# Performance work log

Hardware: AMD Instinct MI355X
Metric: run time of the kernel (lower is better)

## Reference

```python
import jax, jax.numpy as jnp
import numpy as np

N_NODES = 100000
N_EDGES = 1600000
IN_F, HID_F, OUT_F = 128, 128, 64


def _sage_conv(x, src, dst, W_self, W_neigh, b, n_nodes):
    # DGL SAGEConv 'mean': out = x @ W_self + mean_{u in N(v)} x_u @ W_neigh + b
    agg = jax.ops.segment_sum(x[src], dst, num_segments=n_nodes)  # [N, d]
    deg = jax.ops.segment_sum(jnp.ones_like(dst, dtype=x.dtype), dst, num_segments=n_nodes)
    neigh = agg / jnp.maximum(deg, 1.0)[:, None]  # zero-in-degree nodes -> 0
    return x @ W_self + neigh @ W_neigh + b


def setup_inputs() -> dict:
    key = jax.random.key(0)
    ks = jax.random.split(key, 8)
    return {
        "features": jax.random.normal(ks[0], (N_NODES, IN_F), dtype=jnp.float32),
        "edge_src": jax.random.randint(ks[1], (N_EDGES,), 0, N_NODES, dtype=jnp.int32),
        "edge_dst": jax.random.randint(ks[2], (N_EDGES,), 0, N_NODES, dtype=jnp.int32),
        "W1_self": jax.random.normal(ks[3], (IN_F, HID_F), dtype=jnp.float32) / np.sqrt(IN_F),
        "W1_neigh": jax.random.normal(ks[4], (IN_F, HID_F), dtype=jnp.float32) / np.sqrt(IN_F),
        "b1": jnp.zeros((HID_F,), dtype=jnp.float32),
        "W2_self": jax.random.normal(ks[5], (HID_F, OUT_F), dtype=jnp.float32) / np.sqrt(HID_F),
        "W2_neigh": jax.random.normal(ks[6], (HID_F, OUT_F), dtype=jnp.float32) / np.sqrt(HID_F),
        "b2": jnp.zeros((OUT_F,), dtype=jnp.float32),
    }


def reference(features, edge_src, edge_dst, W1_self, W1_neigh, b1, W2_self, W2_neigh, b2):
    n = features.shape[0]
    x = _sage_conv(features, edge_src, edge_dst, W1_self, W1_neigh, b1, n)
    x = jax.nn.relu(x)
    # dropout with training=False is a no-op
    return _sage_conv(x, edge_src, edge_dst, W2_self, W2_neigh, b2, n)
```

## Files before the change

kernel.cpp:

```cpp
#include <hip/hip_runtime.h>

#define NODES 100000
#define EDGES 1600000
#define BSH 8
#define NBUCK ((NODES + 255) >> BSH)
#define CHUNK 4096
#define LMAX 8192
#define MCHUNKS ((NODES + 31) / 32)
#define CONVB 12500
#define MLPGRID 512

using bf16x8 = __attribute__((ext_vector_type(8))) short;
using f32x4  = __attribute__((ext_vector_type(4))) float;
using f32x2  = __attribute__((ext_vector_type(2))) float;

__device__ __forceinline__ unsigned short f2b(float f) {
    unsigned u = __builtin_bit_cast(unsigned, f);
    unsigned r = (u + 0x7FFFu + ((u >> 16) & 1u)) >> 16;
    return (unsigned short)r;
}

__device__ __forceinline__ f32x2 pkadd(f32x2 a, f32x2 b) {
    f32x2 d;
    asm("v_pk_add_f32 %0, %1, %2" : "=v"(d) : "v"(a), "v"(b));
    return d;
}
__device__ __forceinline__ f32x2 pkfma(f32x2 a, f32x2 b, f32x2 c) {
    f32x2 d;
    asm("v_pk_fma_f32 %0, %1, %2, %3" : "=v"(d) : "v"(a), "v"(b), "v"(c));
    return d;
}
__device__ __forceinline__ unsigned cvt2bf(float lo, float hi) {
    unsigned r;
    asm("v_cvt_pk_bf16_f32 %0, %1, %2" : "=v"(r) : "v"(lo), "v"(hi));
    return r;
}

__device__ __forceinline__ bf16x8 gl16(const unsigned short* p) {
    bf16x8 r;
    asm volatile("global_load_dwordx4 %0, %1, off" : "=&v"(r) : "v"(p));
    return r;
}

__device__ __forceinline__ void addpk8(f32x2* a, uint2 v) {
    a[0] = pkadd(a[0], __builtin_amdgcn_cvt_pk_f32_fp8((int)v.x, false));
    a[1] = pkadd(a[1], __builtin_amdgcn_cvt_pk_f32_fp8((int)v.x, true));
    a[2] = pkadd(a[2], __builtin_amdgcn_cvt_pk_f32_fp8((int)v.y, false));
    a[3] = pkadd(a[3], __builtin_amdgcn_cvt_pk_f32_fp8((int)v.y, true));
}


__global__ __launch_bounds__(256) void conv_hist(
    const float* __restrict__ in, unsigned short* __restrict__ outb,
    unsigned char* __restrict__ outq, int n4,
    const float* __restrict__ W1s, const float* __restrict__ W1n,
    const float* __restrict__ W2s, const float* __restrict__ W2n,
    unsigned short* __restrict__ Wt1s, unsigned short* __restrict__ Wt1n,
    unsigned short* __restrict__ Wt2s, unsigned short* __restrict__ Wt2n,
    const int* __restrict__ dst, int* __restrict__ bucket_cnt) {
    int t = threadIdx.x;
    if (blockIdx.x < CONVB) {
        int i = blockIdx.x * 256 + t;
        if (i < n4) {
            float4 v = reinterpret_cast<const float4*>(in)[i];
            uint2 o;
            o.x = (unsigned)f2b(v.x) | ((unsigned)f2b(v.y) << 16);
            o.y = (unsigned)f2b(v.z) | ((unsigned)f2b(v.w) << 16);
            reinterpret_cast<uint2*>(outb)[i] = o;
            int pk = __builtin_amdgcn_cvt_pk_fp8_f32(v.x, v.y, 0, false);
            pk = __builtin_amdgcn_cvt_pk_fp8_f32(v.z, v.w, pk, true);
            reinterpret_cast<unsigned*>(outq)[i] = (unsigned)pk;
        }
        if (i < 16384) {
            int k = i >> 7, n = i & 127;
            Wt1s[n * 128 + k] = f2b(W1s[i]);
            Wt1n[n * 128 + k] = f2b(W1n[i]);
        }
        if (i < 8192) {
            int k = i >> 6, n = i & 63;
            Wt2s[n * 128 + k] = f2b(W2s[i]);
            Wt2n[n * 128 + k] = f2b(W2n[i]);
        }
        return;
    }
    __shared__ int lcnt[512];
    lcnt[t] = 0; lcnt[t + 256] = 0;
    __syncthreads();
    int base = (blockIdx.x - CONVB) * 16384;
    int n = EDGES - base;
    if (n > 16384) n = 16384;
    const int4* d4 = reinterpret_cast<const int4*>(dst + base);
    for (int i = t; i < (n >> 2); i += 256) {
        int4 d = d4[i];
        atomicAdd(&lcnt[d.x >> BSH], 1);
        atomicAdd(&lcnt[d.y >> BSH], 1);
        atomicAdd(&lcnt[d.z >> BSH], 1);
        atomicAdd(&lcnt[d.w >> BSH], 1);
    }
    for (int i = (n & ~3) + t; i < n; i += 256) atomicAdd(&lcnt[dst[base + i] >> BSH], 1);
    __syncthreads();
    if (lcnt[t]) atomicAdd(&bucket_cnt[t], lcnt[t]);
    if (lcnt[t + 256]) atomicAdd(&bucket_cnt[t + 256], lcnt[t + 256]);
}

__global__ void bscan_kernel(const int* __restrict__ bucket_cnt, int* __restrict__ bucket_off,
                             int* __restrict__ gcursor, int* __restrict__ row_ptr) {
    __shared__ int sh[512];
    int t = threadIdx.x;
    int v = (t < NBUCK) ? bucket_cnt[t] : 0;
    sh[t] = v;
    __syncthreads();
    for (int off = 1; off < 512; off <<= 1) {
        int x = (t >= off) ? sh[t - off] : 0;
        __syncthreads();
        sh[t] += x;
        __syncthreads();
    }
    int excl = sh[t] - v;
    if (t < NBUCK) { bucket_off[t] = excl; gcursor[t] = excl; }
    if (t == NBUCK) bucket_off[t] = EDGES;
    if (t == 0) row_ptr[NODES] = EDGES;
}

__global__ __launch_bounds__(256) void binscat_kernel(
    const int* __restrict__ src, const int* __restrict__ dst,
    int* __restrict__ gcursor, unsigned* __restrict__ pairs) {
    __shared__ int cnt[512];
    __shared__ int scn[512];
    __shared__ int gbs[512];
    __shared__ int cur[512];
    __shared__ uint2 stage[CHUNK];
    int t = threadIdx.x;
    int base = blockIdx.x * CHUNK;
    int n = EDGES - base;
    if (n > CHUNK) n = CHUNK;

    cnt[t] = 0; cnt[t + 256] = 0;
    __syncthreads();

    uint2 my[16];
#pragma unroll
    for (int i = 0; i < 16; ++i) {
        int idx = t + i * 256;
        if (idx < n) {
            int d = dst[base + idx];
            int s = src[base + idx];
            my[i] = make_uint2((unsigned)d, (unsigned)s);
            atomicAdd(&cnt[d >> BSH], 1);
        } else {
            my[i] = make_uint2(0xFFFFFFFFu, 0);
        }
    }
    __syncthreads();
    scn[t] = cnt[t]; scn[t + 256] = cnt[t + 256];
    __syncthreads();
    for (int off = 1; off < 512; off <<= 1) {
        int a0 = (t >= off) ? scn[t - off] : 0;
        int a1 = (t + 256 >= off) ? scn[t + 256 - off] : 0;
        __syncthreads();
        scn[t] += a0; scn[t + 256] += a1;
        __syncthreads();
    }
    cur[t] = scn[t] - cnt[t];
    cur[t + 256] = scn[t + 256] - cnt[t + 256];
    __syncthreads();
#pragma unroll
    for (int i = 0; i < 16; ++i) {
        if (my[i].x != 0xFFFFFFFFu) {
            int b = (int)(my[i].x >> BSH);
            int p = atomicAdd(&cur[b], 1);
            stage[p] = my[i];
        }
    }
    for (int b2 = t; b2 < 512; b2 += 256) {
        int c = cnt[b2];
        gbs[b2] = (c > 0 && b2 < NBUCK) ? atomicAdd(&gcursor[b2], c) : 0;
    }
    __syncthreads();
    for (int idx = t; idx < n; idx += 256) {
        uint2 p = stage[idx];
        int b = (int)(p.x >> BSH);
        int excl = scn[b] - cnt[b];
        pairs[gbs[b] + idx - excl] = ((p.x & 255u) << 24) | p.y;
    }
}

__global__ __launch_bounds__(256) void localsort_kernel(
    const unsigned* __restrict__ pairs, const int* __restrict__ bucket_off,
    int* __restrict__ row_ptr, int* __restrict__ src_sorted) {
    __shared__ int cnt[256];
    __shared__ int cur[256];
    __shared__ int stage[LMAX];
    int b = blockIdx.x;
    int t = threadIdx.x;
    int node0 = b << BSH;
    int pbeg = bucket_off[b], pend = bucket_off[b + 1];
    int n = pend - pbeg;
    cnt[t] = 0;
    __syncthreads();
    for (int e = pbeg + t; e < pend; e += 256)
        atomicAdd(&cnt[(int)(pairs[e] >> 24)], 1);
    __syncthreads();
    int v = cnt[t];
    cur[t] = v;
    __syncthreads();
    for (int off = 1; off < 256; off <<= 1) {
        int x = (t >= off) ? cur[t - off] : 0;
        __syncthreads();
        cur[t] += x;
        __syncthreads();
    }
    int excl = cur[t] - v;
    int node = node0 + t;
    if (node < NODES) row_ptr[node] = pbeg + excl;
    cur[t] = excl;
    __syncthreads();
    if (n <= LMAX) {
        for (int e = pbeg + t; e < pend; e += 256) {
            unsigned p = pairs[e];
            int pos = atomicAdd(&cur[(int)(p >> 24)], 1);
            stage[pos] = (int)(p & 0xFFFFFFu);
        }
        __syncthreads();
        for (int i = t; i < n; i += 256) src_sorted[pbeg + i] = stage[i];
    } else {
        for (int e = pbeg + t; e < pend; e += 256) {
            unsigned p = pairs[e];
            int pos = atomicAdd(&cur[(int)(p >> 24)], 1);
            src_sorted[pbeg + pos] = (int)(p & 0xFFFFFFu);
        }
    }
}


__global__ __launch_bounds__(256) void agg128_fp8(
    const unsigned char* __restrict__ xq, const int* __restrict__ row_ptr,
    const int* __restrict__ srcs, unsigned short* __restrict__ out) {
    int wave = (blockIdx.x * 256 + threadIdx.x) >> 6;
    int lane = threadIdx.x & 63;
    int sl = lane & 15;
    int n = wave * 4 + (lane >> 4);
    if (n >= NODES) return;
    int beg = row_ptr[n], end = row_ptr[n + 1];
    int gb = lane & 48;

    f32x2 A0[4], A1[4];
#pragma unroll
    for (int i = 0; i < 4; ++i) { A0[i] = {0.f, 0.f}; A1[i] = {0.f, 0.f}; }

    const unsigned char* xs = xq + sl * 8;
    for (int base = beg; base < end; base += 16) {
        int idx = base + sl;
        int sv = (idx < end) ? srcs[idx] : NODES;
        uint2 vv[8], ww[8];
#pragma unroll
        for (int j = 0; j < 8; ++j) {
            int s = __shfl(sv, gb + j, 64);
            vv[j] = *reinterpret_cast<const uint2*>(xs + (size_t)s * 128);
        }
#pragma unroll
        for (int j = 0; j < 8; ++j) {
            int s = __shfl(sv, gb + 8 + j, 64);
            ww[j] = *reinterpret_cast<const uint2*>(xs + (size_t)s * 128);
        }
#pragma unroll
        for (int j = 0; j < 8; ++j) addpk8((j & 1) ? A1 : A0, vv[j]);
#pragma unroll
        for (int j = 0; j < 8; ++j) addpk8((j & 1) ? A0 : A1, ww[j]);
    }

    float inv = 1.0f / fmaxf((float)(end - beg), 1.0f);
    f32x2 iv = {inv, inv};
    f32x2 z = {0.f, 0.f};
    f32x2 r0 = pkfma(pkadd(A0[0], A1[0]), iv, z);
    f32x2 r1 = pkfma(pkadd(A0[1], A1[1]), iv, z);
    f32x2 r2 = pkfma(pkadd(A0[2], A1[2]), iv, z);
    f32x2 r3 = pkfma(pkadd(A0[3], A1[3]), iv, z);
    uint4 o;
    o.x = cvt2bf(r0[0], r0[1]);
    o.y = cvt2bf(r1[0], r1[1]);
    o.z = cvt2bf(r2[0], r2[1]);
    o.w = cvt2bf(r3[0], r3[1]);
    *reinterpret_cast<uint4*>(out + (size_t)n * 128 + sl * 8) = o;
}

__global__ __launch_bounds__(256) void agg64_add8(
    const unsigned char* __restrict__ xq, const int* __restrict__ row_ptr,
    const int* __restrict__ srcs, float* __restrict__ out) {
    int wave = (blockIdx.x * 256 + threadIdx.x) >> 6;
    int lane = threadIdx.x & 63;
    int sl = lane & 7;
    int n = wave * 8 + (lane >> 3);
    if (n >= NODES) return;
    int beg = row_ptr[n], end = row_ptr[n + 1];
    int gb = lane & 56;

    f32x2 A0[4], A1[4];
#pragma unroll
    for (int i = 0; i < 4; ++i) { A0[i] = {0.f, 0.f}; A1[i] = {0.f, 0.f}; }

    const unsigned char* xs = xq + sl * 8;
    for (int base = beg; base < end; base += 8) {
        int idx = base + sl;
        int sv = (idx < end) ? srcs[idx] : NODES;
        uint2 vv[8];
#pragma unroll
        for (int j = 0; j < 8; ++j) {
            int s = __shfl(sv, gb + j, 64);
            vv[j] = *reinterpret_cast<const uint2*>(xs + (size_t)s * 64);
        }
#pragma unroll
        for (int j = 0; j < 8; ++j) addpk8((j & 1) ? A1 : A0, vv[j]);
    }

    float inv = 1.0f / fmaxf((float)(end - beg), 1.0f);
    f32x2 iv = {inv, inv};
    float* op = out + (size_t)n * 64 + sl * 8;
    f32x2 r0 = *reinterpret_cast<f32x2*>(op);
    f32x2 r1 = *reinterpret_cast<f32x2*>(op + 2);
    f32x2 r2 = *reinterpret_cast<f32x2*>(op + 4);
    f32x2 r3 = *reinterpret_cast<f32x2*>(op + 6);
    r0 = pkfma(pkadd(A0[0], A1[0]), iv, r0);
    r1 = pkfma(pkadd(A0[1], A1[1]), iv, r1);
    r2 = pkfma(pkadd(A0[2], A1[2]), iv, r2);
    r3 = pkfma(pkadd(A0[3], A1[3]), iv, r3);
    *reinterpret_cast<f32x2*>(op) = r0;
    *reinterpret_cast<f32x2*>(op + 2) = r1;
    *reinterpret_cast<f32x2*>(op + 4) = r2;
    *reinterpret_cast<f32x2*>(op + 6) = r3;
}


__global__ __launch_bounds__(256, 2) void fused_mlp(
    const unsigned short* __restrict__ featb, const unsigned short* __restrict__ agg,
    const unsigned short* __restrict__ Wt1s, const unsigned short* __restrict__ Wt1n,
    const float* __restrict__ b1, const unsigned short* __restrict__ Wt2s,
    const unsigned short* __restrict__ Wt2n, const float* __restrict__ b2,
    unsigned char* __restrict__ x1h8, float* __restrict__ outp) {
    __shared__ __align__(16) unsigned short w1t[32768];
    __shared__ __align__(16) unsigned short x1t[32 * 136];
    int wid = threadIdx.x >> 6, lane = threadIdx.x & 63;
    int l15 = lane & 15, quad = lane >> 4;

    {
        const uint4* gs = reinterpret_cast<const uint4*>(Wt1s);
        const uint4* gn = reinterpret_cast<const uint4*>(Wt1n);
        uint4* ls = reinterpret_cast<uint4*>(w1t);
        uint4* ln = reinterpret_cast<uint4*>(w1t) + 2048;
#pragma unroll
        for (int i = 0; i < 8; ++i) {
            int g = threadIdx.x + i * 256;
            int sw = (g & ~15) | ((g & 15) ^ ((g >> 4) & 7));
            ls[sw] = gs[g];
            ln[sw] = gn[g];
        }
    }

    int col2 = wid * 16 + l15;
    bf16x8 B2s[4], B2n[4];
#pragma unroll
    for (int k = 0; k < 4; ++k) {
        B2s[k] = gl16(Wt2s + (size_t)col2 * 128 + k * 32 + quad * 8);
        B2n[k] = gl16(Wt2n + (size_t)col2 * 128 + k * 32 + quad * 8);
    }
    float bv1[2];
    bv1[0] = b1[wid * 32 + l15];
    bv1[1] = b1[wid * 32 + 16 + l15];
    float bv2 = b2[col2];

    auto loadA = [&](int cc, bf16x8 (&Afd)[2][4], bf16x8 (&Aad)[2][4]) {
#pragma unroll
        for (int rg = 0; rg < 2; ++rg) {
            int r = cc * 32 + rg * 16 + l15;
            const unsigned short* fp = featb + (size_t)r * 128 + quad * 8;
            const unsigned short* ap = agg + (size_t)r * 128 + quad * 8;
#pragma unroll
            for (int k = 0; k < 4; ++k) {
                Afd[rg][k] = *reinterpret_cast<const bf16x8*>(fp + k * 32);
                Aad[rg][k] = *reinterpret_cast<const bf16x8*>(ap + k * 32);
            }
        }
    };

    bf16x8 Af[2][4], Aa[2][4];
    int c = blockIdx.x;
    if (c < MCHUNKS) loadA(c, Af, Aa);

    asm volatile("s_waitcnt vmcnt(0)" ::: "memory");
    __builtin_amdgcn_sched_barrier(0);
    __syncthreads();

    int swz = l15 & 7;
    const unsigned short* wb0 = w1t + (size_t)(wid * 32 + l15) * 128;
    const unsigned short* wb1 = w1t + (size_t)(wid * 32 + 16 + l15) * 128;

    for (; c < MCHUNKS; c += MLPGRID) {
        int rbase = c * 32;
        int cn = c + MLPGRID;

        f32x4 acc[2][2];
#pragma unroll
        for (int rg = 0; rg < 2; ++rg)
#pragma unroll
            for (int nt = 0; nt < 2; ++nt) acc[rg][nt] = {0.f, 0.f, 0.f, 0.f};
#pragma unroll
        for (int k = 0; k < 4; ++k) {
            int so = ((k * 4 + quad) ^ swz) << 3;
            bf16x8 b1s0 = *reinterpret_cast<const bf16x8*>(wb0 + so);
            bf16x8 b1n0 = *reinterpret_cast<const bf16x8*>(wb0 + 16384 + so);
            bf16x8 b1s1 = *reinterpret_cast<const bf16x8*>(wb1 + so);
            bf16x8 b1n1 = *reinterpret_cast<const bf16x8*>(wb1 + 16384 + so);
#pragma unroll
            for (int rg = 0; rg < 2; ++rg) {
                acc[rg][0] = __builtin_amdgcn_mfma_f32_16x16x32_bf16(Af[rg][k], b1s0, acc[rg][0], 0, 0, 0);
                acc[rg][0] = __builtin_amdgcn_mfma_f32_16x16x32_bf16(Aa[rg][k], b1n0, acc[rg][0], 0, 0, 0);
                acc[rg][1] = __builtin_amdgcn_mfma_f32_16x16x32_bf16(Af[rg][k], b1s1, acc[rg][1], 0, 0, 0);
                acc[rg][1] = __builtin_amdgcn_mfma_f32_16x16x32_bf16(Aa[rg][k], b1n1, acc[rg][1], 0, 0, 0);
            }
        }

        bf16x8 Pf[2][4], Pa[2][4];
        if (cn < MCHUNKS) loadA(cn, Pf, Pa);

#pragma unroll
        for (int nt = 0; nt < 2; ++nt)
#pragma unroll
            for (int rg = 0; rg < 2; ++rg)
#pragma unroll
                for (int rr = 0; rr < 4; ++rr) {
                    float v = fmaxf(acc[rg][nt][rr] + bv1[nt], 0.f);
                    x1t[(rg * 16 + quad * 4 + rr) * 136 + wid * 32 + nt * 16 + l15] = f2b(v);
                }
        __syncthreads();

        f32x4 acc2s[2], acc2n[2];
#pragma unroll
        for (int rg = 0; rg < 2; ++rg) { acc2s[rg] = {0.f, 0.f, 0.f, 0.f}; acc2n[rg] = {0.f, 0.f, 0.f, 0.f}; }
#pragma unroll
        for (int k = 0; k < 4; ++k)
#pragma unroll
            for (int rg = 0; rg < 2; ++rg) {
                bf16x8 a = *reinterpret_cast<const bf16x8*>(&x1t[(rg * 16 + l15) * 136 + k * 32 + quad * 8]);
                acc2s[rg] = __builtin_amdgcn_mfma_f32_16x16x32_bf16(a, B2s[k], acc2s[rg], 0, 0, 0);
                acc2n[rg] = __builtin_amdgcn_mfma_f32_16x16x32_bf16(a, B2n[k], acc2n[rg], 0, 0, 0);
            }
        __syncthreads();

#pragma unroll
        for (int rg = 0; rg < 2; ++rg)
#pragma unroll
            for (int rr = 0; rr < 4; ++rr) {
                int row = rbase + rg * 16 + quad * 4 + rr;
                float vn = acc2n[rg][rr];
                int pk = __builtin_amdgcn_cvt_pk_fp8_f32(vn, vn, 0, false);
                x1h8[(size_t)row * 64 + col2] = (unsigned char)(pk & 0xFF);
                outp[(size_t)row * 64 + col2] = acc2s[rg][rr] + bv2;
            }

        if (cn < MCHUNKS) {
#pragma unroll
            for (int rg = 0; rg < 2; ++rg)
#pragma unroll
                for (int k = 0; k < 4; ++k) {
                    Af[rg][k] = Pf[rg][k];
                    Aa[rg][k] = Pa[rg][k];
                }
        }
    }
}


extern "C" void kernel_launch(void* const* d_in, const int* in_sizes, int n_in,
                              void* d_out, int out_size, void* d_ws, size_t ws_size,
                              hipStream_t stream) {
    const float* features = (const float*)d_in[0];
    const int* esrc = (const int*)d_in[1];
    const int* edst = (const int*)d_in[2];
    const float* W1s = (const float*)d_in[3];
    const float* W1n = (const float*)d_in[4];
    const float* b1  = (const float*)d_in[5];
    const float* W2s = (const float*)d_in[6];
    const float* W2n = (const float*)d_in[7];
    const float* b2  = (const float*)d_in[8];
    float* out = (float*)d_out;

    char* ws = (char*)d_ws;
    size_t off = 0;
    auto alloc = [&](size_t bytes) {
        void* p = ws + off;
        off += (bytes + 255) & ~(size_t)255;
        return p;
    };
    int* bucket_cnt = (int*)alloc(512 * 4);
    int* bucket_off = (int*)alloc(512 * 4);
    int* gcursor    = (int*)alloc(512 * 4);
    int* row_ptr    = (int*)alloc((size_t)(NODES + 1) * 4);
    int* src_sorted = (int*)alloc((size_t)EDGES * 4);
    unsigned* pairs = (unsigned*)alloc((size_t)EDGES * 4);
    unsigned short* featb = (unsigned short*)alloc((size_t)NODES * 128 * 2);
    unsigned char*  feat8 = (unsigned char*)alloc((size_t)(NODES + 1) * 128);
    unsigned short* agg1  = (unsigned short*)alloc((size_t)NODES * 128 * 2);
    unsigned char*  x1h8  = (unsigned char*)alloc((size_t)(NODES + 1) * 64);
    unsigned short* Wt1s  = (unsigned short*)alloc(16384 * 2);
    unsigned short* Wt1n  = (unsigned short*)alloc(16384 * 2);
    unsigned short* Wt2s  = (unsigned short*)alloc(8192 * 2);
    unsigned short* Wt2n  = (unsigned short*)alloc(8192 * 2);

    hipMemsetAsync(bucket_cnt, 0, 512 * 4, stream);
    hipMemsetAsync(feat8 + (size_t)NODES * 128, 0, 128, stream);
    hipMemsetAsync(x1h8 + (size_t)NODES * 64, 0, 64, stream);

    conv_hist<<<CONVB + (EDGES + 16383) / 16384, 256, 0, stream>>>(
        features, featb, feat8, NODES * 128 / 4, W1s, W1n, W2s, W2n,
        Wt1s, Wt1n, Wt2s, Wt2n, edst, bucket_cnt);

    bscan_kernel<<<1, 512, 0, stream>>>(bucket_cnt, bucket_off, gcursor, row_ptr);
    binscat_kernel<<<(EDGES + CHUNK - 1) / CHUNK, 256, 0, stream>>>(esrc, edst, gcursor, pairs);
    localsort_kernel<<<NBUCK, 256, 0, stream>>>(pairs, bucket_off, row_ptr, src_sorted);

    agg128_fp8<<<(NODES / 4 * 64 + 255) / 256, 256, 0, stream>>>(feat8, row_ptr, src_sorted, agg1);

    fused_mlp<<<MLPGRID, 256, 0, stream>>>(featb, agg1, Wt1s, Wt1n, b1, Wt2s, Wt2n, b2, x1h8, out);

    agg64_add8<<<(NODES / 8 * 64 + 255) / 256, 256, 0, stream>>>(x1h8, row_ptr, src_sorted, out);
}
```

Before: 255.8 us.

## Split fused two-layer MLP kernel into separate layer kernels via global bf16 buffer

Splits the fused MLP kernel into two kernels. The first computes the layer-1 hidden activations and writes them to a new global bf16 buffer. The second reads that buffer, computes the layer-2 self and neighbor projections, and prefetches the next chunk in registers. This removes the shared-memory round trip and the block barriers inside the loop, and lets the second layer use a larger grid and higher occupancy. In exchange it adds an extra ~25MB of global write and read traffic plus one more kernel launch.

```diff
diff --git a/kernel.cpp b/kernel.cpp
--- a/kernel.cpp
+++ b/kernel.cpp
@@ -8,7 +8,8 @@
 #define LMAX 8192
 #define MCHUNKS ((NODES + 31) / 32)
 #define CONVB 12500
-#define MLPGRID 512
+#define MLP1GRID 512
+#define MLP2GRID 1024
 
 using bf16x8 = __attribute__((ext_vector_type(8))) short;
 using f32x4  = __attribute__((ext_vector_type(4))) float;
@@ -331,14 +332,11 @@
 }
 
 
-__global__ __launch_bounds__(256, 2) void fused_mlp(
+__global__ __launch_bounds__(256, 2) void mlp1(
     const unsigned short* __restrict__ featb, const unsigned short* __restrict__ agg,
     const unsigned short* __restrict__ Wt1s, const unsigned short* __restrict__ Wt1n,
-    const float* __restrict__ b1, const unsigned short* __restrict__ Wt2s,
-    const unsigned short* __restrict__ Wt2n, const float* __restrict__ b2,
-    unsigned char* __restrict__ x1h8, float* __restrict__ outp) {
+    const float* __restrict__ b1, unsigned short* __restrict__ x1b) {
     __shared__ __align__(16) unsigned short w1t[32768];
-    __shared__ __align__(16) unsigned short x1t[32 * 136];
     int wid = threadIdx.x >> 6, lane = threadIdx.x & 63;
     int l15 = lane & 15, quad = lane >> 4;
 
@@ -355,18 +353,9 @@
             ln[sw] = gn[g];
         }
     }
-
-    int col2 = wid * 16 + l15;
-    bf16x8 B2s[4], B2n[4];
-#pragma unroll
-    for (int k = 0; k < 4; ++k) {
-        B2s[k] = gl16(Wt2s + (size_t)col2 * 128 + k * 32 + quad * 8);
-        B2n[k] = gl16(Wt2n + (size_t)col2 * 128 + k * 32 + quad * 8);
-    }
     float bv1[2];
     bv1[0] = b1[wid * 32 + l15];
     bv1[1] = b1[wid * 32 + 16 + l15];
-    float bv2 = b2[col2];
 
     auto loadA = [&](int cc, bf16x8 (&Afd)[2][4], bf16x8 (&Aad)[2][4]) {
 #pragma unroll
@@ -385,18 +374,15 @@
     bf16x8 Af[2][4], Aa[2][4];
     int c = blockIdx.x;
     if (c < MCHUNKS) loadA(c, Af, Aa);
-
-    asm volatile("s_waitcnt vmcnt(0)" ::: "memory");
-    __builtin_amdgcn_sched_barrier(0);
     __syncthreads();
 
     int swz = l15 & 7;
     const unsigned short* wb0 = w1t + (size_t)(wid * 32 + l15) * 128;
     const unsigned short* wb1 = w1t + (size_t)(wid * 32 + 16 + l15) * 128;
 
-    for (; c < MCHUNKS; c += MLPGRID) {
+    for (; c < MCHUNKS; c += MLP1GRID) {
         int rbase = c * 32;
-        int cn = c + MLPGRID;
+        int cn = c + MLP1GRID;
 
         f32x4 acc[2][2];
 #pragma unroll
@@ -429,9 +415,59 @@
 #pragma unroll
                 for (int rr = 0; rr < 4; ++rr) {
                     float v = fmaxf(acc[rg][nt][rr] + bv1[nt], 0.f);
-                    x1t[(rg * 16 + quad * 4 + rr) * 136 + wid * 32 + nt * 16 + l15] = f2b(v);
+                    int row = rbase + rg * 16 + quad * 4 + rr;
+                    x1b[(size_t)row * 128 + wid * 32 + nt * 16 + l15] = f2b(v);
                 }
-        __syncthreads();
+
+        if (cn < MCHUNKS) {
+#pragma unroll
+            for (int rg = 0; rg < 2; ++rg)
+#pragma unroll
+                for (int k = 0; k < 4; ++k) {
+                    Af[rg][k] = Pf[rg][k];
+                    Aa[rg][k] = Pa[rg][k];
+                }
+        }
+    }
+}
+
+
+__global__ __launch_bounds__(256, 3) void mlp2(
+    const unsigned short* __restrict__ x1b,
+    const unsigned short* __restrict__ Wt2s, const unsigned short* __restrict__ Wt2n,
+    const float* __restrict__ b2,
+    unsigned char* __restrict__ x1h8, float* __restrict__ outp) {
+    int wid = threadIdx.x >> 6, lane = threadIdx.x & 63;
+    int l15 = lane & 15, quad = lane >> 4;
+    int col2 = wid * 16 + l15;
+
+    bf16x8 B2s[4], B2n[4];
+#pragma unroll
+    for (int k = 0; k < 4; ++k) {
+        B2s[k] = gl16(Wt2s + (size_t)col2 * 128 + k * 32 + quad * 8);
+        B2n[k] = gl16(Wt2n + (size_t)col2 * 128 + k * 32 + quad * 8);
+    }
+    float bv2 = b2[col2];
+    asm volatile("s_waitcnt vmcnt(0)" ::: "memory");
+    __builtin_amdgcn_sched_barrier(0);
+
+    auto loadA = [&](int cc, bf16x8 (&Ad)[2][4]) {
+#pragma unroll
+        for (int rg = 0; rg < 2; ++rg) {
+            int r = cc * 32 + rg * 16 + l15;
+            const unsigned short* xp = x1b + (size_t)r * 128 + quad * 8;
+#pragma unroll
+            for (int k = 0; k < 4; ++k) Ad[rg][k] = *reinterpret_cast<const bf16x8*>(xp + k * 32);
+        }
+    };
+
+    bf16x8 A[2][4];
+    int c = blockIdx.x;
+    if (c < MCHUNKS) loadA(c, A);
+
+    for (; c < MCHUNKS; c += MLP2GRID) {
+        int rbase = c * 32;
+        int cn = c + MLP2GRID;
 
         f32x4 acc2s[2], acc2n[2];
 #pragma unroll
@@ -440,11 +476,12 @@
         for (int k = 0; k < 4; ++k)
 #pragma unroll
             for (int rg = 0; rg < 2; ++rg) {
-                bf16x8 a = *reinterpret_cast<const bf16x8*>(&x1t[(rg * 16 + l15) * 136 + k * 32 + quad * 8]);
-                acc2s[rg] = __builtin_amdgcn_mfma_f32_16x16x32_bf16(a, B2s[k], acc2s[rg], 0, 0, 0);
-                acc2n[rg] = __builtin_amdgcn_mfma_f32_16x16x32_bf16(a, B2n[k], acc2n[rg], 0, 0, 0);
+                acc2s[rg] = __builtin_amdgcn_mfma_f32_16x16x32_bf16(A[rg][k], B2s[k], acc2s[rg], 0, 0, 0);
+                acc2n[rg] = __builtin_amdgcn_mfma_f32_16x16x32_bf16(A[rg][k], B2n[k], acc2n[rg], 0, 0, 0);
             }
-        __syncthreads();
+
+        bf16x8 P[2][4];
+        if (cn < MCHUNKS) loadA(cn, P);
 
 #pragma unroll
         for (int rg = 0; rg < 2; ++rg)
@@ -461,10 +498,7 @@
 #pragma unroll
             for (int rg = 0; rg < 2; ++rg)
 #pragma unroll
-                for (int k = 0; k < 4; ++k) {
-                    Af[rg][k] = Pf[rg][k];
-                    Aa[rg][k] = Pa[rg][k];
-                }
+                for (int k = 0; k < 4; ++k) A[rg][k] = P[rg][k];
         }
     }
 }
@@ -500,6 +534,7 @@
     unsigned short* featb = (unsigned short*)alloc((size_t)NODES * 128 * 2);
     unsigned char*  feat8 = (unsigned char*)alloc((size_t)(NODES + 1) * 128);
     unsigned short* agg1  = (unsigned short*)alloc((size_t)NODES * 128 * 2);
+    unsigned short* x1b   = (unsigned short*)alloc((size_t)NODES * 128 * 2);
     unsigned char*  x1h8  = (unsigned char*)alloc((size_t)(NODES + 1) * 64);
     unsigned short* Wt1s  = (unsigned short*)alloc(16384 * 2);
     unsigned short* Wt1n  = (unsigned short*)alloc(16384 * 2);
@@ -520,7 +555,8 @@
 
     agg128_fp8<<<(NODES / 4 * 64 + 255) / 256, 256, 0, stream>>>(feat8, row_ptr, src_sorted, agg1);
 
-    fused_mlp<<<MLPGRID, 256, 0, stream>>>(featb, agg1, Wt1s, Wt1n, b1, Wt2s, Wt2n, b2, x1h8, out);
+    mlp1<<<MLP1GRID, 256, 0, stream>>>(featb, agg1, Wt1s, Wt1n, b1, x1b);
+    mlp2<<<MLP2GRID, 256, 0, stream>>>(x1b, Wt2s, Wt2n, b2, x1h8, out);
 
     agg64_add8<<<(NODES / 8 * 64 + 255) / 256, 256, 0, stream>>>(x1h8, row_ptr, src_sorted, out);
 }
```

Result: slower. 267.2 us (+4.5%).

## Retile fused MLP to 64-row chunks and unroll gather loop by 16 edges

Applied to the files above, without the earlier changes.

The fused MLP now processes 64-row chunks. Each wave owns 16 rows and computes all 128 hidden columns, where before the wave split by column over 32 rows. The x1 LDS tile uses an XOR swizzle in place of padding, and tail rows are clamped or guarded. The layer-2 aggregation gathers 16 neighbours per iteration so more loads are in flight. In exchange, each wave reads more weight data from LDS per MFMA and uses more registers, which may lower occupancy.

```diff
diff --git a/kernel.cpp b/kernel.cpp
--- a/kernel.cpp
+++ b/kernel.cpp
@@ -6,7 +6,7 @@
 #define NBUCK ((NODES + 255) >> BSH)
 #define CHUNK 4096
 #define LMAX 8192
-#define MCHUNKS ((NODES + 31) / 32)
+#define NCH64 ((NODES + 63) / 64)
 #define CONVB 12500
 #define MLPGRID 512
 
@@ -300,17 +300,23 @@
     for (int i = 0; i < 4; ++i) { A0[i] = {0.f, 0.f}; A1[i] = {0.f, 0.f}; }
 
     const unsigned char* xs = xq + sl * 8;
-    for (int base = beg; base < end; base += 8) {
-        int idx = base + sl;
-        int sv = (idx < end) ? srcs[idx] : NODES;
-        uint2 vv[8];
+    for (int base = beg; base < end; base += 16) {
+        int i0 = base + sl, i1 = base + 8 + sl;
+        int sv0 = (i0 < end) ? srcs[i0] : NODES;
+        int sv1 = (i1 < end) ? srcs[i1] : NODES;
+        uint2 vv[16];
 #pragma unroll
         for (int j = 0; j < 8; ++j) {
-            int s = __shfl(sv, gb + j, 64);
+            int s = __shfl(sv0, gb + j, 64);
             vv[j] = *reinterpret_cast<const uint2*>(xs + (size_t)s * 64);
         }
 #pragma unroll
-        for (int j = 0; j < 8; ++j) addpk8((j & 1) ? A1 : A0, vv[j]);
+        for (int j = 0; j < 8; ++j) {
+            int s = __shfl(sv1, gb + j, 64);
+            vv[8 + j] = *reinterpret_cast<const uint2*>(xs + (size_t)s * 64);
+        }
+#pragma unroll
+        for (int j = 0; j < 16; ++j) addpk8((j & 1) ? A1 : A0, vv[j]);
     }
 
     float inv = 1.0f / fmaxf((float)(end - beg), 1.0f);
@@ -338,7 +344,7 @@
     const unsigned short* __restrict__ Wt2n, const float* __restrict__ b2,
     unsigned char* __restrict__ x1h8, float* __restrict__ outp) {
     __shared__ __align__(16) unsigned short w1t[32768];
-    __shared__ __align__(16) unsigned short x1t[32 * 136];
+    __shared__ __align__(16) unsigned short x1t[64 * 128];
     int wid = threadIdx.x >> 6, lane = threadIdx.x & 63;
     int l15 = lane & 15, quad = lane >> 4;
 
@@ -346,7 +352,7 @@
         const uint4* gs = reinterpret_cast<const uint4*>(Wt1s);
         const uint4* gn = reinterpret_cast<const uint4*>(Wt1n);
         uint4* ls = reinterpret_cast<uint4*>(w1t);
-        uint4* ln = reinterpret_cast<uint4*>(w1t) + 2048;
+        uint4* ln = ls + 2048;
 #pragma unroll
         for (int i = 0; i < 8; ++i) {
             int g = threadIdx.x + i * 256;
@@ -363,108 +369,102 @@
         B2s[k] = gl16(Wt2s + (size_t)col2 * 128 + k * 32 + quad * 8);
         B2n[k] = gl16(Wt2n + (size_t)col2 * 128 + k * 32 + quad * 8);
     }
-    float bv1[2];
-    bv1[0] = b1[wid * 32 + l15];
-    bv1[1] = b1[wid * 32 + 16 + l15];
     float bv2 = b2[col2];
-
-    auto loadA = [&](int cc, bf16x8 (&Afd)[2][4], bf16x8 (&Aad)[2][4]) {
-#pragma unroll
-        for (int rg = 0; rg < 2; ++rg) {
-            int r = cc * 32 + rg * 16 + l15;
-            const unsigned short* fp = featb + (size_t)r * 128 + quad * 8;
-            const unsigned short* ap = agg + (size_t)r * 128 + quad * 8;
-#pragma unroll
-            for (int k = 0; k < 4; ++k) {
-                Afd[rg][k] = *reinterpret_cast<const bf16x8*>(fp + k * 32);
-                Aad[rg][k] = *reinterpret_cast<const bf16x8*>(ap + k * 32);
-            }
+    float bv1[8];
+#pragma unroll
+    for (int nt = 0; nt < 8; ++nt) bv1[nt] = b1[nt * 16 + l15];
+
+    auto loadA = [&](int cc, bf16x8 (&Afd)[4], bf16x8 (&Aad)[4]) {
+        int r = cc * 64 + wid * 16 + l15;
+        if (r >= NODES) r = NODES - 1;
+        const unsigned short* fp = featb + (size_t)r * 128 + quad * 8;
+        const unsigned short* ap = agg + (size_t)r * 128 + quad * 8;
+#pragma unroll
+        for (int k = 0; k < 4; ++k) {
+            Afd[k] = *reinterpret_cast<const bf16x8*>(fp + k * 32);
+            Aad[k] = *reinterpret_cast<const bf16x8*>(ap + k * 32);
         }
     };
 
-    bf16x8 Af[2][4], Aa[2][4];
+    bf16x8 Af[4], Aa[4];
     int c = blockIdx.x;
-    if (c < MCHUNKS) loadA(c, Af, Aa);
+    if (c < NCH64) loadA(c, Af, Aa);
 
     asm volatile("s_waitcnt vmcnt(0)" ::: "memory");
     __builtin_amdgcn_sched_barrier(0);
     __syncthreads();
 
     int swz = l15 & 7;
-    const unsigned short* wb0 = w1t + (size_t)(wid * 32 + l15) * 128;
-    const unsigned short* wb1 = w1t + (size_t)(wid * 32 + 16 + l15) * 128;
-
-    for (; c < MCHUNKS; c += MLPGRID) {
-        int rbase = c * 32;
+
+    for (; c < NCH64; c += MLPGRID) {
+        int rbase = c * 64;
         int cn = c + MLPGRID;
 
-        f32x4 acc[2][2];
-#pragma unroll
-        for (int rg = 0; rg < 2; ++rg)
-#pragma unroll
-            for (int nt = 0; nt < 2; ++nt) acc[rg][nt] = {0.f, 0.f, 0.f, 0.f};
+        f32x4 acc[8];
+#pragma unroll
+        for (int nt = 0; nt < 8; ++nt) acc[nt] = {0.f, 0.f, 0.f, 0.f};
 #pragma unroll
         for (int k = 0; k < 4; ++k) {
             int so = ((k * 4 + quad) ^ swz) << 3;
-            bf16x8 b1s0 = *reinterpret_cast<const bf16x8*>(wb0 + so);
-            bf16x8 b1n0 = *reinterpret_cast<const bf16x8*>(wb0 + 16384 + so);
-            bf16x8 b1s1 = *reinterpret_cast<const bf16x8*>(wb1 + so);
-            bf16x8 b1n1 = *reinterpret_cast<const bf16x8*>(wb1 + 16384 + so);
-#pragma unroll
-            for (int rg = 0; rg < 2; ++rg) {
-                acc[rg][0] = __builtin_amdgcn_mfma_f32_16x16x32_bf16(Af[rg][k], b1s0, acc[rg][0], 0, 0, 0);
-                acc[rg][0] = __builtin_amdgcn_mfma_f32_16x16x32_bf16(Aa[rg][k], b1n0, acc[rg][0], 0, 0, 0);
-                acc[rg][1] = __builtin_amdgcn_mfma_f32_16x16x32_bf16(Af[rg][k], b1s1, acc[rg][1], 0, 0, 0);
-                acc[rg][1] = __builtin_amdgcn_mfma_f32_16x16x32_bf16(Aa[rg][k], b1n1, acc[rg][1], 0, 0, 0);
+#pragma unroll
+            for (int nt = 0; nt < 8; ++nt) {
+                const unsigned short* wb = w1t + (size_t)(nt * 16 + l15) * 128;
+                bf16x8 b1s = *reinterpret_cast<const bf16x8*>(wb + so);
+                bf16x8 b1n = *reinterpret_cast<const bf16x8*>(wb + 16384 + so);
+                acc[nt] = __builtin_amdgcn_mfma_f32_16x16x32_bf16(Af[k], b1s, acc[nt], 0, 0, 0);
+                acc[nt] = __builtin_amdgcn_mfma_f32_16x16x32_bf16(Aa[k], b1n, acc[nt], 0, 0, 0);
             }
         }
 
-        bf16x8 Pf[2][4], Pa[2][4];
-        if (cn < MCHUNKS) loadA(cn, Pf, Pa);
-
-#pragma unroll
-        for (int nt = 0; nt < 2; ++nt)
-#pragma unroll
-            for (int rg = 0; rg < 2; ++rg)
-#pragma unroll
-                for (int rr = 0; rr < 4; ++rr) {
-                    float v = fmaxf(acc[rg][nt][rr] + bv1[nt], 0.f);
-                    x1t[(rg * 16 + quad * 4 + rr) * 136 + wid * 32 + nt * 16 + l15] = f2b(v);
+        bf16x8 Pf[4], Pa[4];
+        if (cn < NCH64) loadA(cn, Pf, Pa);
+
+#pragma unroll
+        for (int nt = 0; nt < 8; ++nt)
+#pragma unroll
+            for (int rr = 0; rr < 4; ++rr) {
+                float v = fmaxf(acc[nt][rr] + bv1[nt], 0.f);
+                int row = wid * 16 + quad * 4 + rr;
+                int col = nt * 16 + l15;
+                int slot = (col >> 3) ^ (row & 7);
+                x1t[row * 128 + slot * 8 + (col & 7)] = f2b(v);
+            }
+        __syncthreads();
+
+        f32x4 a2s[4], a2n[4];
+#pragma unroll
+        for (int mt = 0; mt < 4; ++mt) { a2s[mt] = {0.f, 0.f, 0.f, 0.f}; a2n[mt] = {0.f, 0.f, 0.f, 0.f}; }
+#pragma unroll
+        for (int k = 0; k < 4; ++k)
+#pragma unroll
+            for (int mt = 0; mt < 4; ++mt) {
+                int row = mt * 16 + l15;
+                int slot = (k * 4 + quad) ^ (row & 7);
+                bf16x8 a = *reinterpret_cast<const bf16x8*>(x1t + row * 128 + slot * 8);
+                a2s[mt] = __builtin_amdgcn_mfma_f32_16x16x32_bf16(a, B2s[k], a2s[mt], 0, 0, 0);
+                a2n[mt] = __builtin_amdgcn_mfma_f32_16x16x32_bf16(a, B2n[k], a2n[mt], 0, 0, 0);
+            }
+        __syncthreads();
+
+#pragma unroll
+        for (int mt = 0; mt < 4; ++mt)
+#pragma unroll
+            for (int rr = 0; rr < 4; ++rr) {
+                int row = rbase + mt * 16 + quad * 4 + rr;
+                if (row < NODES) {
+                    float vn = a2n[mt][rr];
+                    int pk = __builtin_amdgcn_cvt_pk_fp8_f32(vn, vn, 0, false);
+                    x1h8[(size_t)row * 64 + col2] = (unsigned char)(pk & 0xFF);
+                    outp[(size_t)row * 64 + col2] = a2s[mt][rr] + bv2;
                 }
-        __syncthreads();
-
-        f32x4 acc2s[2], acc2n[2];
-#pragma unroll
-        for (int rg = 0; rg < 2; ++rg) { acc2s[rg] = {0.f, 0.f, 0.f, 0.f}; acc2n[rg] = {0.f, 0.f, 0.f, 0.f}; }
-#pragma unroll
-        for (int k = 0; k < 4; ++k)
-#pragma unroll
-            for (int rg = 0; rg < 2; ++rg) {
-                bf16x8 a = *reinterpret_cast<const bf16x8*>(&x1t[(rg * 16 + l15) * 136 + k * 32 + quad * 8]);
-                acc2s[rg] = __builtin_amdgcn_mfma_f32_16x16x32_bf16(a, B2s[k], acc2s[rg], 0, 0, 0);
-                acc2n[rg] = __builtin_amdgcn_mfma_f32_16x16x32_bf16(a, B2n[k], acc2n[rg], 0, 0, 0);
             }
-        __syncthreads();
-
-#pragma unroll
-        for (int rg = 0; rg < 2; ++rg)
-#pragma unroll
-            for (int rr = 0; rr < 4; ++rr) {
-                int row = rbase + rg * 16 + quad * 4 + rr;
-                float vn = acc2n[rg][rr];
-                int pk = __builtin_amdgcn_cvt_pk_fp8_f32(vn, vn, 0, false);
-                x1h8[(size_t)row * 64 + col2] = (unsigned char)(pk & 0xFF);
-                outp[(size_t)row * 64 + col2] = acc2s[rg][rr] + bv2;
+
+        if (cn < NCH64) {
+#pragma unroll
+            for (int k = 0; k < 4; ++k) {
+                Af[k] = Pf[k];
+                Aa[k] = Pa[k];
             }
-
-        if (cn < MCHUNKS) {
-#pragma unroll
-            for (int rg = 0; rg < 2; ++rg)
-#pragma unroll
-                for (int k = 0; k < 4; ++k) {
-                    Af[rg][k] = Pf[rg][k];
-                    Aa[rg][k] = Pa[rg][k];
-                }
         }
     }
 }
```

Measured after the change: 237.4 us. 7.2% less time.
